# Optimization experiments

Hardware: AMD Instinct MI355X
Metric: run time of the kernel (lower is better)

The kernel has to match this reference:

```python
import jax, jax.numpy as jnp
import numpy as np

N = 20000        # nodes
E = 640000       # edges (before self-loops)
F_IN = 128
HID = 64
HEADS = 4
F_OUT = 128
G = 64           # graphs in batch
NEG_SLOPE = 0.2  # PyG GATConv leaky_relu default


def setup_inputs() -> dict:
    key = jax.random.key(0)
    ks = jax.random.split(key, 16)
    s = 0.05
    x = jax.random.normal(ks[0], (N, F_IN), jnp.float32)
    edge_index = jax.random.randint(ks[1], (2, E), 0, N, dtype=jnp.int64)
    batch = jnp.sort(jax.random.randint(ks[2], (N,), 0, G, dtype=jnp.int64))
    # layer 1: F_IN -> HID x HEADS (concat)
    W1 = jax.random.normal(ks[3], (F_IN, HEADS * HID), jnp.float32) * s
    a_src1 = jax.random.normal(ks[4], (HEADS, HID), jnp.float32) * s
    a_dst1 = jax.random.normal(ks[5], (HEADS, HID), jnp.float32) * s
    b1 = jnp.zeros((HEADS * HID,), jnp.float32)
    # layer 2: HEADS*HID -> HID x HEADS (concat)
    W2 = jax.random.normal(ks[6], (HEADS * HID, HEADS * HID), jnp.float32) * s
    a_src2 = jax.random.normal(ks[7], (HEADS, HID), jnp.float32) * s
    a_dst2 = jax.random.normal(ks[8], (HEADS, HID), jnp.float32) * s
    b2 = jnp.zeros((HEADS * HID,), jnp.float32)
    # layer 3: HEADS*HID -> F_OUT, heads=1, concat=False (mean)
    W3 = jax.random.normal(ks[9], (HEADS * HID, F_OUT), jnp.float32) * s
    a_src3 = jax.random.normal(ks[10], (1, F_OUT), jnp.float32) * s
    a_dst3 = jax.random.normal(ks[11], (1, F_OUT), jnp.float32) * s
    b3 = jnp.zeros((F_OUT,), jnp.float32)
    return dict(x=x, edge_index=edge_index, batch=batch,
                W1=W1, a_src1=a_src1, a_dst1=a_dst1, b1=b1,
                W2=W2, a_src2=a_src2, a_dst2=a_dst2, b2=b2,
                W3=W3, a_src3=a_src3, a_dst3=a_dst3, b3=b3)


def _gat_layer(x, src, dst, W, a_s, a_d, b, heads, concat):
    n = x.shape[0]
    h = (x @ W).reshape(n, heads, -1)                # [N,H,C]
    alpha_s = (h * a_s[None]).sum(-1)                # [N,H]
    alpha_d = (h * a_d[None]).sum(-1)                # [N,H]
    e = jax.nn.leaky_relu(alpha_s[src] + alpha_d[dst], NEG_SLOPE)  # [E,H]
    # segment softmax over incoming edges of each dst node
    m = jax.ops.segment_max(e, dst, num_segments=n)
    ex = jnp.exp(e - m[dst])
    denom = jax.ops.segment_sum(ex, dst, num_segments=n)
    alpha = ex / (denom[dst] + 1e-16)                # [E,H]
    out = jax.ops.segment_sum(alpha[:, :, None] * h[src], dst, num_segments=n)  # [N,H,C]
    out = out.reshape(n, -1) if concat else out.mean(axis=1)
    return out + b


def reference(x, edge_index, batch, W1, a_src1, a_dst1, b1,
              W2, a_src2, a_dst2, b2, W3, a_src3, a_dst3, b3):
    n = x.shape[0]
    # add self loops (PyG GATConv default add_self_loops=True)
    loop = jnp.arange(n, dtype=edge_index.dtype)
    src = jnp.concatenate([edge_index[0], loop])
    dst = jnp.concatenate([edge_index[1], loop])

    h = _gat_layer(x, src, dst, W1, a_src1, a_dst1, b1, HEADS, True)
    h = jax.nn.elu(h)
    h = _gat_layer(h, src, dst, W2, a_src2, a_dst2, b2, HEADS, True)
    h = jax.nn.elu(h)
    h = _gat_layer(h, src, dst, W3, a_src3, a_dst3, b3, 1, False)

    # global mean pool over graphs
    sums = jax.ops.segment_sum(h, batch, num_segments=G)
    cnts = jax.ops.segment_sum(jnp.ones((n, 1), h.dtype), batch, num_segments=G)
    graph_embedding = sums / jnp.maximum(cnts, 1.0)
    return graph_embedding, h
```

## Files before the change

kernel.cpp:

```cpp
#include <hip/hip_runtime.h>
#include <hip/hip_bf16.h>
#include <math.h>

#define N_NODES 20000
#define N_EDGES 640000
#define ET_EDGES (N_EDGES + N_NODES)
#define G_GRAPHS 64
#define NEG_SLOPE 0.2f

typedef __attribute__((ext_vector_type(8))) short s8v;
typedef __attribute__((ext_vector_type(4))) float f4v;

__device__ __forceinline__ unsigned short bf_hi(float f) {
    union { float f; unsigned int u; } c; c.f = f;
    unsigned int r = (c.u + 0x7fffu + ((c.u >> 16) & 1u)) >> 16;
    return (unsigned short)r;
}
__device__ __forceinline__ float bf_f(unsigned short h) {
    union { unsigned int u; float f; } c; c.u = ((unsigned int)h) << 16;
    return c.f;
}


__global__ void hist_dst(const int* __restrict__ ei, int* __restrict__ cnt,
                         const int* __restrict__ batch, int* __restrict__ gstart) {
    int j = blockIdx.x * blockDim.x + threadIdx.x;
    if (blockIdx.x == 0 && threadIdx.x <= G_GRAPHS) {
        int g = threadIdx.x;
        int lo = 0, hi = N_NODES;
        while (lo < hi) {
            int mid = (lo + hi) >> 1;
            if (batch[mid] < g) lo = mid + 1; else hi = mid;
        }
        gstart[g] = lo;
    }
    if (j >= ET_EDGES) return;
    int d = (j < N_EDGES) ? ei[N_EDGES + j] : (j - N_EDGES);
    atomicAdd(&cnt[d], 1);
}

__global__ __launch_bounds__(1024) void scan_rowptr(const int* __restrict__ cnt,
                                                    int* __restrict__ row_ptr) {
    __shared__ int sums[1024];
    const int n = N_NODES;
    const int CH = (n + 1023) / 1024;
    int t = threadIdx.x;
    int base = t * CH;
    int s = 0;
    for (int i = 0; i < CH; ++i) {
        int idx = base + i;
        if (idx < n) s += cnt[idx];
    }
    sums[t] = s;
    __syncthreads();
    for (int o = 1; o < 1024; o <<= 1) {
        int v = (t >= o) ? sums[t - o] : 0;
        __syncthreads();
        sums[t] += v;
        __syncthreads();
    }
    int run = (t == 0) ? 0 : sums[t - 1];
    for (int i = 0; i < CH; ++i) {
        int idx = base + i;
        if (idx < n) { row_ptr[idx] = run; run += cnt[idx]; }
    }
    if (t == 1023) row_ptr[n] = sums[1023];
}

__global__ void fill_csr(const int* __restrict__ ei, const int* __restrict__ row_ptr,
                         int* __restrict__ cur, int* __restrict__ col) {
    int j = blockIdx.x * blockDim.x + threadIdx.x;
    if (j >= ET_EDGES) return;
    int s, d;
    if (j < N_EDGES) { s = ei[j]; d = ei[N_EDGES + j]; }
    else             { s = d = j - N_EDGES; }
    int pos = row_ptr[d] + atomicAdd(&cur[d], 1);
    col[pos] = s;
}


__global__ void split_f32(const float* __restrict__ in, unsigned short* __restrict__ hi,
                          unsigned short* __restrict__ lo, int n) {
    int i = (blockIdx.x * blockDim.x + threadIdx.x) * 4;
    if (i >= n) return;
    float4 v = *(const float4*)&in[i];
    ushort4 h, l;
    h.x = bf_hi(v.x); l.x = bf_hi(v.x - bf_f(h.x));
    h.y = bf_hi(v.y); l.y = bf_hi(v.y - bf_f(h.y));
    h.z = bf_hi(v.z); l.z = bf_hi(v.z - bf_f(h.z));
    h.w = bf_hi(v.w); l.w = bf_hi(v.w - bf_f(h.w));
    *(ushort4*)&hi[i] = h;
    *(ushort4*)&lo[i] = l;
}

__global__ void wsplit(const float* __restrict__ W, unsigned short* __restrict__ th,
                       unsigned short* __restrict__ tl, int K, int Nc) {
    int idx = blockIdx.x * blockDim.x + threadIdx.x;
    if (idx >= K * Nc) return;
    int k = idx / Nc, n = idx % Nc;
    float v = W[idx];
    unsigned short h = bf_hi(v);
    th[n * K + k] = h;
    tl[n * K + k] = bf_hi(v - bf_f(h));
}


#define LDT 40

__global__ __launch_bounds__(256) void gemm_split(
        const unsigned short* __restrict__ Ah, const unsigned short* __restrict__ Al,
        const unsigned short* __restrict__ Bh, const unsigned short* __restrict__ Bl,
        float* __restrict__ C, int M, int Nc, int K) {
    __shared__ unsigned short lAh[128 * LDT];
    __shared__ unsigned short lAl[128 * LDT];
    __shared__ unsigned short lBh[64 * LDT];
    __shared__ unsigned short lBl[64 * LDT];
    int bm = blockIdx.x * 128, bn = blockIdx.y * 64;
    int t = threadIdx.x, w = t >> 6, lane = t & 63;
    int wm = (w >> 1) * 64, wn = (w & 1) * 32;

    f4v acc[4][2] = {};

    int sr = t >> 1, sk = (t & 1) << 4;
    int br = t >> 2, bk = (t & 3) << 3;
    int ar = bm + sr; if (ar >= M) ar = M - 1;
    const unsigned short* pAh = Ah + (size_t)ar * K + sk;
    const unsigned short* pAl = Al + (size_t)ar * K + sk;
    const unsigned short* pBh = Bh + (size_t)(bn + br) * K + bk;
    const unsigned short* pBl = Bl + (size_t)(bn + br) * K + bk;

    int fr = lane & 15, fk = (lane >> 4) << 3;

    for (int k0 = 0; k0 < K; k0 += 32) {
        uint4 vh0 = *(const uint4*)(pAh + k0);
        uint4 vh1 = *(const uint4*)(pAh + k0 + 8);
        uint4 vl0 = *(const uint4*)(pAl + k0);
        uint4 vl1 = *(const uint4*)(pAl + k0 + 8);
        uint4 wh  = *(const uint4*)(pBh + k0);
        uint4 wl  = *(const uint4*)(pBl + k0);
        __syncthreads();
        *(uint4*)&lAh[sr * LDT + sk]     = vh0;
        *(uint4*)&lAh[sr * LDT + sk + 8] = vh1;
        *(uint4*)&lAl[sr * LDT + sk]     = vl0;
        *(uint4*)&lAl[sr * LDT + sk + 8] = vl1;
        *(uint4*)&lBh[br * LDT + bk] = wh;
        *(uint4*)&lBl[br * LDT + bk] = wl;
        __syncthreads();

        s8v a_h[4], a_l[4], b_h[2], b_l[2];
        #pragma unroll
        for (int mi = 0; mi < 4; ++mi) {
            a_h[mi] = *(const s8v*)&lAh[(wm + mi * 16 + fr) * LDT + fk];
            a_l[mi] = *(const s8v*)&lAl[(wm + mi * 16 + fr) * LDT + fk];
        }
        #pragma unroll
        for (int nj = 0; nj < 2; ++nj) {
            b_h[nj] = *(const s8v*)&lBh[(wn + nj * 16 + fr) * LDT + fk];
            b_l[nj] = *(const s8v*)&lBl[(wn + nj * 16 + fr) * LDT + fk];
        }
        #pragma unroll
        for (int mi = 0; mi < 4; ++mi)
            #pragma unroll
            for (int nj = 0; nj < 2; ++nj) {
                acc[mi][nj] = __builtin_amdgcn_mfma_f32_16x16x32_bf16(
                    a_h[mi], b_h[nj], acc[mi][nj], 0, 0, 0);
                acc[mi][nj] = __builtin_amdgcn_mfma_f32_16x16x32_bf16(
                    a_h[mi], b_l[nj], acc[mi][nj], 0, 0, 0);
                acc[mi][nj] = __builtin_amdgcn_mfma_f32_16x16x32_bf16(
                    a_l[mi], b_h[nj], acc[mi][nj], 0, 0, 0);
            }
    }

    #pragma unroll
    for (int mi = 0; mi < 4; ++mi)
        #pragma unroll
        for (int nj = 0; nj < 2; ++nj) {
            int row0 = bm + wm + mi * 16 + (lane >> 4) * 4;
            int colc = bn + wn + nj * 16 + (lane & 15);
            #pragma unroll
            for (int q = 0; q < 4; ++q) {
                int r = row0 + q;
                if (r < M) C[(size_t)r * Nc + colc] = acc[mi][nj][q];
            }
        }
}


template <int HEADS, int C>
__global__ __launch_bounds__(256) void node_alpha2(const float* __restrict__ h,
                                                   const float* __restrict__ a_src,
                                                   const float* __restrict__ a_dst,
                                                   float* __restrict__ asT,
                                                   float* __restrict__ adT) {
    constexpr int F = HEADS * C;
    constexpr int VEC = F / 64;
    constexpr int LPH = C / VEC;
    int wid = threadIdx.x >> 6, lane = threadIdx.x & 63;
    int v = blockIdx.x * 4 + wid;
    if (v >= N_NODES) return;
    const float* hp = h + (size_t)v * F + lane * VEC;
    float ps = 0.f, pd = 0.f;
    #pragma unroll
    for (int c = 0; c < VEC; ++c) {
        float hv = hp[c];
        ps = fmaf(hv, a_src[lane * VEC + c], ps);
        pd = fmaf(hv, a_dst[lane * VEC + c], pd);
    }
    #pragma unroll
    for (int o = LPH / 2; o; o >>= 1) {
        ps += __shfl_xor(ps, o);
        pd += __shfl_xor(pd, o);
    }
    if ((lane & (LPH - 1)) == 0) {
        int head = lane / LPH;
        asT[head * N_NODES + v] = ps;
        adT[head * N_NODES + v] = pd;
    }
}


template <int NSLICE, int SCH, int F, int HEADS, bool DO_ELU, bool SPLIT>
__global__ __launch_bounds__(256) void gat_aggregate_sliced(
        const float* __restrict__ h,
        const float* __restrict__ asT,
        const float* __restrict__ adT,
        const int* __restrict__ row_ptr,
        const int* __restrict__ col,
        const float* __restrict__ bias,
        float* __restrict__ out,
        unsigned short* __restrict__ oh,
        unsigned short* __restrict__ ol) {
    constexpr int CL = SCH / 4;
    constexpr int E  = 64 / CL;
    constexpr int CPH = F / HEADS;
    __shared__ int   s_off[4][64];
    __shared__ float s_p[4][64];
    int slice = blockIdx.x & (NSLICE - 1);
    int ng = blockIdx.x >> 2;
    int wid = threadIdx.x >> 6, lane = threadIdx.x & 63;
    int v = ng * 4 + wid;
    if (v >= N_NODES) return;
    int head = (slice * SCH) / CPH;
    int eg = lane / CL, cl = lane % CL;
    int r0 = row_ptr[v], r1 = row_ptr[v + 1];
    float ad = adT[head * N_NODES + v];
    const float* asrc = asT + head * N_NODES;
    float acc[4] = {};
    float lsum = 0.f;
    const char* hb = (const char*)(h + slice * SCH + cl * 4);

#define GATHER4(gg)                                                        \
    {                                                                      \
        int k0 = ((gg) + 0) * E + eg;                                      \
        int k1 = ((gg) + 1) * E + eg;                                      \
        int k2 = ((gg) + 2) * E + eg;                                      \
        int k3 = ((gg) + 3) * E + eg;                                      \
        float p0 = s_p[wid][k0]; int o0 = s_off[wid][k0];                  \
        float p1 = s_p[wid][k1]; int o1 = s_off[wid][k1];                  \
        float p2 = s_p[wid][k2]; int o2 = s_off[wid][k2];                  \
        float p3 = s_p[wid][k3]; int o3 = s_off[wid][k3];                  \
        float4 h0 = *(const float4*)(hb + o0);                             \
        float4 h1 = *(const float4*)(hb + o1);                             \
        float4 h2 = *(const float4*)(hb + o2);                             \
        float4 h3 = *(const float4*)(hb + o3);                             \
        acc[0] = fmaf(p0, h0.x, acc[0]);                                   \
        acc[1] = fmaf(p0, h0.y, acc[1]);                                   \
        acc[2] = fmaf(p0, h0.z, acc[2]);                                   \
        acc[3] = fmaf(p0, h0.w, acc[3]);                                   \
        acc[0] = fmaf(p1, h1.x, acc[0]);                                   \
        acc[1] = fmaf(p1, h1.y, acc[1]);                                   \
        acc[2] = fmaf(p1, h1.z, acc[2]);                                   \
        acc[3] = fmaf(p1, h1.w, acc[3]);                                   \
        acc[0] = fmaf(p2, h2.x, acc[0]);                                   \
        acc[1] = fmaf(p2, h2.y, acc[1]);                                   \
        acc[2] = fmaf(p2, h2.z, acc[2]);                                   \
        acc[3] = fmaf(p2, h2.w, acc[3]);                                   \
        acc[0] = fmaf(p3, h3.x, acc[0]);                                   \
        acc[1] = fmaf(p3, h3.y, acc[1]);                                   \
        acc[2] = fmaf(p3, h3.z, acc[2]);                                   \
        acc[3] = fmaf(p3, h3.w, acc[3]);                                   \
    }

    for (int base = r0; base < r1; base += 64) {
        int j = base + lane;
        bool valid = j < r1;
        int s = col[valid ? j : r0];
        float e = asrc[s] + ad;
        e = (e > 0.f) ? e : NEG_SLOPE * e;
        float p = valid ? __expf(e) : 0.f;
        lsum += p;
        s_p[wid][lane] = p;
        s_off[wid][lane] = s * (F * 4);

        int nk = min(64, r1 - base);
        int nkg = (nk + E - 1) / E;
        int g = 0;
        for (; g + 4 <= nkg; g += 4) GATHER4(g);
        if (g < nkg) GATHER4(g);
    }
#undef GATHER4

    #pragma unroll
    for (int o = 32; o; o >>= 1) lsum += __shfl_xor(lsum, o);
    #pragma unroll
    for (int c = 0; c < 4; ++c) {
        #pragma unroll
        for (int o = CL; o < 64; o <<= 1) acc[c] += __shfl_xor(acc[c], o);
    }
    if (eg == 0) {
        float inv = 1.f / (lsum + 1e-16f);
        int ch0 = slice * SCH + cl * 4;
        float o4[4];
        #pragma unroll
        for (int c = 0; c < 4; ++c) {
            float o = acc[c] * inv + bias[ch0 + c];
            if (DO_ELU) o = (o > 0.f) ? o : expm1f(o);
            o4[c] = o;
        }
        if (SPLIT) {
            ushort4 hv, lv;
            hv.x = bf_hi(o4[0]); lv.x = bf_hi(o4[0] - bf_f(hv.x));
            hv.y = bf_hi(o4[1]); lv.y = bf_hi(o4[1] - bf_f(hv.y));
            hv.z = bf_hi(o4[2]); lv.z = bf_hi(o4[2] - bf_f(hv.z));
            hv.w = bf_hi(o4[3]); lv.w = bf_hi(o4[3] - bf_f(hv.w));
            *(ushort4*)&oh[(size_t)v * F + ch0] = hv;
            *(ushort4*)&ol[(size_t)v * F + ch0] = lv;
        } else {
            *(float4*)&out[(size_t)v * F + ch0] =
                make_float4(o4[0], o4[1], o4[2], o4[3]);
        }
    }
}


__global__ void pool_mean4(const float* __restrict__ hout, const int* __restrict__ gstart,
                           float* __restrict__ gout) {
    int g = blockIdx.x;
    int q = blockIdx.y;
    int c = threadIdx.x;
    int off = gstart[g], end = gstart[g + 1];
    float inv = 1.f / fmaxf((float)(end - off), 1.0f);
    float s = 0.f;
    for (int i = off + q; i < end; i += 4) s += hout[(size_t)i * 128 + c];
    atomicAdd(&gout[g * 128 + c], s * inv);
}


static inline size_t align_up(size_t x, size_t a) { return (x + a - 1) & ~(a - 1); }

extern "C" void kernel_launch(void* const* d_in, const int* in_sizes, int n_in,
                              void* d_out, int out_size, void* d_ws, size_t ws_size,
                              hipStream_t stream) {
    const float* x   = (const float*)d_in[0];
    const int*   ei  = (const int*)d_in[1];
    const int*   bat = (const int*)d_in[2];
    const float* W1  = (const float*)d_in[3];
    const float* as1 = (const float*)d_in[4];
    const float* ad1 = (const float*)d_in[5];
    const float* b1  = (const float*)d_in[6];
    const float* W2  = (const float*)d_in[7];
    const float* as2 = (const float*)d_in[8];
    const float* ad2 = (const float*)d_in[9];
    const float* b2  = (const float*)d_in[10];
    const float* W3  = (const float*)d_in[11];
    const float* as3 = (const float*)d_in[12];
    const float* ad3 = (const float*)d_in[13];
    const float* b3  = (const float*)d_in[14];

    float* gout = (float*)d_out;
    float* hout = (float*)d_out + G_GRAPHS * 128;

    char* w = (char*)d_ws;
    size_t o = 0;
    float* bufA = (float*)(w + o);           o = align_up(o + (size_t)N_NODES * 256 * 4, 256);
    unsigned short* Bh = (unsigned short*)(w + o); o = align_up(o + (size_t)N_NODES * 256 * 2, 256);
    unsigned short* Bl = (unsigned short*)(w + o); o = align_up(o + (size_t)N_NODES * 256 * 2, 256);
    unsigned short* xh = (unsigned short*)(w + o); o = align_up(o + (size_t)N_NODES * 128 * 2, 256);
    unsigned short* xl = (unsigned short*)(w + o); o = align_up(o + (size_t)N_NODES * 128 * 2, 256);
    unsigned short* Wt1h = (unsigned short*)(w + o); o = align_up(o + (size_t)256 * 128 * 2, 256);
    unsigned short* Wt1l = (unsigned short*)(w + o); o = align_up(o + (size_t)256 * 128 * 2, 256);
    unsigned short* Wt2h = (unsigned short*)(w + o); o = align_up(o + (size_t)256 * 256 * 2, 256);
    unsigned short* Wt2l = (unsigned short*)(w + o); o = align_up(o + (size_t)256 * 256 * 2, 256);
    unsigned short* Wt3h = (unsigned short*)(w + o); o = align_up(o + (size_t)128 * 256 * 2, 256);
    unsigned short* Wt3l = (unsigned short*)(w + o); o = align_up(o + (size_t)128 * 256 * 2, 256);
    float* asv  = (float*)(w + o); o = align_up(o + (size_t)N_NODES * 4 * 4, 256);
    float* adv  = (float*)(w + o); o = align_up(o + (size_t)N_NODES * 4 * 4, 256);
    int* row_ptr = (int*)(w + o);  o = align_up(o + (size_t)(N_NODES + 1) * 4, 256);
    int* col     = (int*)(w + o);  o = align_up(o + (size_t)ET_EDGES * 4, 256);
    int* cnt     = (int*)(w + o);  o += (size_t)N_NODES * 4;
    int* cur     = (int*)(w + o);  o = align_up(o + (size_t)N_NODES * 4, 256);
    int* gstart  = (int*)(w + o);  o = align_up(o + (size_t)(G_GRAPHS + 1) * 4, 256);

    hipMemsetAsync(cnt, 0, (size_t)N_NODES * 8, stream);
    hipMemsetAsync(gout, 0, (size_t)G_GRAPHS * 128 * 4, stream);
    hist_dst<<<(ET_EDGES + 255) / 256, 256, 0, stream>>>(ei, cnt, bat, gstart);
    scan_rowptr<<<1, 1024, 0, stream>>>(cnt, row_ptr);
    fill_csr<<<(ET_EDGES + 255) / 256, 256, 0, stream>>>(ei, row_ptr, cur, col);
    split_f32<<<(N_NODES * 128 / 4 + 255) / 256, 256, 0, stream>>>(x, xh, xl, N_NODES * 128);
    wsplit<<<(128 * 256 + 255) / 256, 256, 0, stream>>>(W1, Wt1h, Wt1l, 128, 256);
    wsplit<<<(256 * 256 + 255) / 256, 256, 0, stream>>>(W2, Wt2h, Wt2l, 256, 256);
    wsplit<<<(256 * 128 + 255) / 256, 256, 0, stream>>>(W3, Wt3h, Wt3l, 256, 128);

    int gm = (N_NODES + 127) / 128;
    int nb = (N_NODES + 3) / 4;
    int nbs = nb * 4;

    gemm_split<<<dim3(gm, 4), 256, 0, stream>>>(xh, xl, Wt1h, Wt1l, bufA, N_NODES, 256, 128);
    node_alpha2<4, 64><<<nb, 256, 0, stream>>>(bufA, as1, ad1, asv, adv);
    gat_aggregate_sliced<4, 64, 256, 4, true, true><<<nbs, 256, 0, stream>>>(
        bufA, asv, adv, row_ptr, col, b1, nullptr, Bh, Bl);

    gemm_split<<<dim3(gm, 4), 256, 0, stream>>>(Bh, Bl, Wt2h, Wt2l, bufA, N_NODES, 256, 256);
    node_alpha2<4, 64><<<nb, 256, 0, stream>>>(bufA, as2, ad2, asv, adv);
    gat_aggregate_sliced<4, 64, 256, 4, true, true><<<nbs, 256, 0, stream>>>(
        bufA, asv, adv, row_ptr, col, b2, nullptr, Bh, Bl);

    gemm_split<<<dim3(gm, 2), 256, 0, stream>>>(Bh, Bl, Wt3h, Wt3l, bufA, N_NODES, 128, 256);
    node_alpha2<1, 128><<<nb, 256, 0, stream>>>(bufA, as3, ad3, asv, adv);
    gat_aggregate_sliced<4, 32, 128, 1, false, false><<<nbs, 256, 0, stream>>>(
        bufA, asv, adv, row_ptr, col, b3, hout, nullptr, nullptr);

    pool_mean4<<<dim3(G_GRAPHS, 4), 128, 0, stream>>>(hout, gstart, gout);
}
```

Before: 433.2 us.

## Split GAT aggregation into 8 channel slices with a fully unrolled 64-edge gather

The aggregation kernels now use 8 channel slices instead of 4, so each block handles half as many channels and twice as many blocks are launched. The per-chunk gather loop is fully unrolled over all 64 shared-memory slots, always issuing CL loads, instead of looping only over the valid edges. Edge probability and offset are packed into one int2 in shared memory. The column reads and the bf16 split-output stores become nontemporal. The aim is more memory-level parallelism and fewer loop-control branches. In exchange, each node's column indices, attention logits and exponentials are recomputed in twice as many blocks, and padded slots issue redundant gathers of the first source row.

```diff
diff --git a/kernel.cpp b/kernel.cpp
--- a/kernel.cpp
+++ b/kernel.cpp
@@ -233,10 +233,9 @@
     constexpr int CL = SCH / 4;
     constexpr int E  = 64 / CL;
     constexpr int CPH = F / HEADS;
-    __shared__ int   s_off[4][64];
-    __shared__ float s_p[4][64];
+    __shared__ int2 s_po[4][64];
     int slice = blockIdx.x & (NSLICE - 1);
-    int ng = blockIdx.x >> 2;
+    int ng = blockIdx.x / NSLICE;
     int wid = threadIdx.x >> 6, lane = threadIdx.x & 63;
     int v = ng * 4 + wid;
     if (v >= N_NODES) return;
@@ -249,56 +248,31 @@
     float lsum = 0.f;
     const char* hb = (const char*)(h + slice * SCH + cl * 4);
 
-#define GATHER4(gg)                                                        \
-    {                                                                      \
-        int k0 = ((gg) + 0) * E + eg;                                      \
-        int k1 = ((gg) + 1) * E + eg;                                      \
-        int k2 = ((gg) + 2) * E + eg;                                      \
-        int k3 = ((gg) + 3) * E + eg;                                      \
-        float p0 = s_p[wid][k0]; int o0 = s_off[wid][k0];                  \
-        float p1 = s_p[wid][k1]; int o1 = s_off[wid][k1];                  \
-        float p2 = s_p[wid][k2]; int o2 = s_off[wid][k2];                  \
-        float p3 = s_p[wid][k3]; int o3 = s_off[wid][k3];                  \
-        float4 h0 = *(const float4*)(hb + o0);                             \
-        float4 h1 = *(const float4*)(hb + o1);                             \
-        float4 h2 = *(const float4*)(hb + o2);                             \
-        float4 h3 = *(const float4*)(hb + o3);                             \
-        acc[0] = fmaf(p0, h0.x, acc[0]);                                   \
-        acc[1] = fmaf(p0, h0.y, acc[1]);                                   \
-        acc[2] = fmaf(p0, h0.z, acc[2]);                                   \
-        acc[3] = fmaf(p0, h0.w, acc[3]);                                   \
-        acc[0] = fmaf(p1, h1.x, acc[0]);                                   \
-        acc[1] = fmaf(p1, h1.y, acc[1]);                                   \
-        acc[2] = fmaf(p1, h1.z, acc[2]);                                   \
-        acc[3] = fmaf(p1, h1.w, acc[3]);                                   \
-        acc[0] = fmaf(p2, h2.x, acc[0]);                                   \
-        acc[1] = fmaf(p2, h2.y, acc[1]);                                   \
-        acc[2] = fmaf(p2, h2.z, acc[2]);                                   \
-        acc[3] = fmaf(p2, h2.w, acc[3]);                                   \
-        acc[0] = fmaf(p3, h3.x, acc[0]);                                   \
-        acc[1] = fmaf(p3, h3.y, acc[1]);                                   \
-        acc[2] = fmaf(p3, h3.z, acc[2]);                                   \
-        acc[3] = fmaf(p3, h3.w, acc[3]);                                   \
-    }
-
     for (int base = r0; base < r1; base += 64) {
         int j = base + lane;
         bool valid = j < r1;
-        int s = col[valid ? j : r0];
+        int s = __builtin_nontemporal_load(&col[valid ? j : r0]);
         float e = asrc[s] + ad;
         e = (e > 0.f) ? e : NEG_SLOPE * e;
         float p = valid ? __expf(e) : 0.f;
         lsum += p;
-        s_p[wid][lane] = p;
-        s_off[wid][lane] = s * (F * 4);
-
-        int nk = min(64, r1 - base);
-        int nkg = (nk + E - 1) / E;
-        int g = 0;
-        for (; g + 4 <= nkg; g += 4) GATHER4(g);
-        if (g < nkg) GATHER4(g);
-    }
-#undef GATHER4
+        s_po[wid][lane] = make_int2(s * (F * 4), __float_as_int(p));
+
+        int2 po[CL];
+        #pragma unroll
+        for (int g = 0; g < CL; ++g) po[g] = s_po[wid][g * E + eg];
+        float4 hv[CL];
+        #pragma unroll
+        for (int g = 0; g < CL; ++g) hv[g] = *(const float4*)(hb + po[g].x);
+        #pragma unroll
+        for (int g = 0; g < CL; ++g) {
+            float pk = __int_as_float(po[g].y);
+            acc[0] = fmaf(pk, hv[g].x, acc[0]);
+            acc[1] = fmaf(pk, hv[g].y, acc[1]);
+            acc[2] = fmaf(pk, hv[g].z, acc[2]);
+            acc[3] = fmaf(pk, hv[g].w, acc[3]);
+        }
+    }
 
     #pragma unroll
     for (int o = 32; o; o >>= 1) lsum += __shfl_xor(lsum, o);
@@ -318,13 +292,16 @@
             o4[c] = o;
         }
         if (SPLIT) {
-            ushort4 hv, lv;
-            hv.x = bf_hi(o4[0]); lv.x = bf_hi(o4[0] - bf_f(hv.x));
-            hv.y = bf_hi(o4[1]); lv.y = bf_hi(o4[1] - bf_f(hv.y));
-            hv.z = bf_hi(o4[2]); lv.z = bf_hi(o4[2] - bf_f(hv.z));
-            hv.w = bf_hi(o4[3]); lv.w = bf_hi(o4[3] - bf_f(hv.w));
-            *(ushort4*)&oh[(size_t)v * F + ch0] = hv;
-            *(ushort4*)&ol[(size_t)v * F + ch0] = lv;
+            ushort4 hv4, lv4;
+            hv4.x = bf_hi(o4[0]); lv4.x = bf_hi(o4[0] - bf_f(hv4.x));
+            hv4.y = bf_hi(o4[1]); lv4.y = bf_hi(o4[1] - bf_f(hv4.y));
+            hv4.z = bf_hi(o4[2]); lv4.z = bf_hi(o4[2] - bf_f(hv4.z));
+            hv4.w = bf_hi(o4[3]); lv4.w = bf_hi(o4[3] - bf_f(hv4.w));
+            unsigned long long hvu, lvu;
+            __builtin_memcpy(&hvu, &hv4, 8);
+            __builtin_memcpy(&lvu, &lv4, 8);
+            __builtin_nontemporal_store(hvu, (unsigned long long*)&oh[(size_t)v * F + ch0]);
+            __builtin_nontemporal_store(lvu, (unsigned long long*)&ol[(size_t)v * F + ch0]);
         } else {
             *(float4*)&out[(size_t)v * F + ch0] =
                 make_float4(o4[0], o4[1], o4[2], o4[3]);
@@ -403,21 +380,21 @@
 
     int gm = (N_NODES + 127) / 128;
     int nb = (N_NODES + 3) / 4;
-    int nbs = nb * 4;
+    int nbs = nb * 8;
 
     gemm_split<<<dim3(gm, 4), 256, 0, stream>>>(xh, xl, Wt1h, Wt1l, bufA, N_NODES, 256, 128);
     node_alpha2<4, 64><<<nb, 256, 0, stream>>>(bufA, as1, ad1, asv, adv);
-    gat_aggregate_sliced<4, 64, 256, 4, true, true><<<nbs, 256, 0, stream>>>(
+    gat_aggregate_sliced<8, 32, 256, 4, true, true><<<nbs, 256, 0, stream>>>(
         bufA, asv, adv, row_ptr, col, b1, nullptr, Bh, Bl);
 
     gemm_split<<<dim3(gm, 4), 256, 0, stream>>>(Bh, Bl, Wt2h, Wt2l, bufA, N_NODES, 256, 256);
     node_alpha2<4, 64><<<nb, 256, 0, stream>>>(bufA, as2, ad2, asv, adv);
-    gat_aggregate_sliced<4, 64, 256, 4, true, true><<<nbs, 256, 0, stream>>>(
+    gat_aggregate_sliced<8, 32, 256, 4, true, true><<<nbs, 256, 0, stream>>>(
         bufA, asv, adv, row_ptr, col, b2, nullptr, Bh, Bl);
 
     gemm_split<<<dim3(gm, 2), 256, 0, stream>>>(Bh, Bl, Wt3h, Wt3l, bufA, N_NODES, 128, 256);
     node_alpha2<1, 128><<<nb, 256, 0, stream>>>(bufA, as3, ad3, asv, adv);
-    gat_aggregate_sliced<4, 32, 128, 1, false, false><<<nbs, 256, 0, stream>>>(
+    gat_aggregate_sliced<8, 16, 128, 1, false, false><<<nbs, 256, 0, stream>>>(
         bufA, asv, adv, row_ptr, col, b3, hout, nullptr, nullptr);
 
     pool_mean4<<<dim3(G_GRAPHS, 4), 128, 0, stream>>>(hout, gstart, gout);
```

Measured after the change: 568.9 us. +31.3%, slower.

## Precompute edge softmax weights in separate pass, fuse prep kernels, unroll gather by 8

Applied to the files above, without the earlier changes.

Folds the x/W bf16 splitting and the memsets into one prep kernel, which cuts launch count. Adds a per-layer edge_alpha pass that computes the exp attention weights and per-node denominators once per edge and stores them in a [head, E] buffer. Before this, each of the 4 channel slices recomputed them. The aggregate kernel now reads those precomputed weights and uses an 8-wide gather unroll. The cost is an extra kernel per layer and extra global traffic for the pex buffer (about 10 MB written and read back per layer).

```diff
diff --git a/kernel.cpp b/kernel.cpp
--- a/kernel.cpp
+++ b/kernel.cpp
@@ -79,29 +79,63 @@
 }
 
 
-__global__ void split_f32(const float* __restrict__ in, unsigned short* __restrict__ hi,
-                          unsigned short* __restrict__ lo, int n) {
-    int i = (blockIdx.x * blockDim.x + threadIdx.x) * 4;
-    if (i >= n) return;
-    float4 v = *(const float4*)&in[i];
-    ushort4 h, l;
-    h.x = bf_hi(v.x); l.x = bf_hi(v.x - bf_f(h.x));
-    h.y = bf_hi(v.y); l.y = bf_hi(v.y - bf_f(h.y));
-    h.z = bf_hi(v.z); l.z = bf_hi(v.z - bf_f(h.z));
-    h.w = bf_hi(v.w); l.w = bf_hi(v.w - bf_f(h.w));
-    *(ushort4*)&hi[i] = h;
-    *(ushort4*)&lo[i] = l;
-}
-
-__global__ void wsplit(const float* __restrict__ W, unsigned short* __restrict__ th,
-                       unsigned short* __restrict__ tl, int K, int Nc) {
+__global__ void prep_split(const float* __restrict__ x,
+                           const float* __restrict__ W1, const float* __restrict__ W2,
+                           const float* __restrict__ W3,
+                           unsigned short* __restrict__ xh, unsigned short* __restrict__ xl,
+                           unsigned short* __restrict__ w1h, unsigned short* __restrict__ w1l,
+                           unsigned short* __restrict__ w2h, unsigned short* __restrict__ w2l,
+                           unsigned short* __restrict__ w3h, unsigned short* __restrict__ w3l,
+                           int* __restrict__ cntcur, float* __restrict__ gout) {
     int idx = blockIdx.x * blockDim.x + threadIdx.x;
-    if (idx >= K * Nc) return;
-    int k = idx / Nc, n = idx % Nc;
-    float v = W[idx];
-    unsigned short h = bf_hi(v);
-    th[n * K + k] = h;
-    tl[n * K + k] = bf_hi(v - bf_f(h));
+    if (idx < 640000) {
+        int i = idx * 4;
+        float4 v = *(const float4*)&x[i];
+        ushort4 h, l;
+        h.x = bf_hi(v.x); l.x = bf_hi(v.x - bf_f(h.x));
+        h.y = bf_hi(v.y); l.y = bf_hi(v.y - bf_f(h.y));
+        h.z = bf_hi(v.z); l.z = bf_hi(v.z - bf_f(h.z));
+        h.w = bf_hi(v.w); l.w = bf_hi(v.w - bf_f(h.w));
+        *(ushort4*)&xh[i] = h;
+        *(ushort4*)&xl[i] = l;
+        return;
+    }
+    idx -= 640000;
+    if (idx < 32768) {
+        int k = idx / 256, n = idx % 256;
+        float v = W1[idx];
+        unsigned short h = bf_hi(v);
+        w1h[n * 128 + k] = h;
+        w1l[n * 128 + k] = bf_hi(v - bf_f(h));
+        return;
+    }
+    idx -= 32768;
+    if (idx < 65536) {
+        int k = idx / 256, n = idx % 256;
+        float v = W2[idx];
+        unsigned short h = bf_hi(v);
+        w2h[n * 256 + k] = h;
+        w2l[n * 256 + k] = bf_hi(v - bf_f(h));
+        return;
+    }
+    idx -= 65536;
+    if (idx < 32768) {
+        int k = idx / 128, n = idx % 128;
+        float v = W3[idx];
+        unsigned short h = bf_hi(v);
+        w3h[n * 256 + k] = h;
+        w3l[n * 256 + k] = bf_hi(v - bf_f(h));
+        return;
+    }
+    idx -= 32768;
+    if (idx < 10000) {
+        *(int4*)&cntcur[idx * 4] = make_int4(0, 0, 0, 0);
+        return;
+    }
+    idx -= 10000;
+    if (idx < 2048) {
+        *(float4*)&gout[idx * 4] = make_float4(0.f, 0.f, 0.f, 0.f);
+    }
 }
 
 
@@ -187,11 +221,11 @@
 
 
 template <int HEADS, int C>
-__global__ __launch_bounds__(256) void node_alpha2(const float* __restrict__ h,
+__global__ __launch_bounds__(256) void node_alpha3(const float* __restrict__ h,
                                                    const float* __restrict__ a_src,
                                                    const float* __restrict__ a_dst,
-                                                   float* __restrict__ asT,
-                                                   float* __restrict__ adT) {
+                                                   float* __restrict__ asi,
+                                                   float* __restrict__ adi) {
     constexpr int F = HEADS * C;
     constexpr int VEC = F / 64;
     constexpr int LPH = C / VEC;
@@ -213,17 +247,67 @@
     }
     if ((lane & (LPH - 1)) == 0) {
         int head = lane / LPH;
-        asT[head * N_NODES + v] = ps;
-        adT[head * N_NODES + v] = pd;
-    }
-}
-
-
-template <int NSLICE, int SCH, int F, int HEADS, bool DO_ELU, bool SPLIT>
-__global__ __launch_bounds__(256) void gat_aggregate_sliced(
+        asi[v * HEADS + head] = ps;
+        adi[v * HEADS + head] = pd;
+    }
+}
+
+
+template <int H>
+__global__ __launch_bounds__(256) void edge_alpha2(
+        const float* __restrict__ asi,
+        const float* __restrict__ adi,
+        const int* __restrict__ row_ptr,
+        const int* __restrict__ col,
+        float* __restrict__ pex,
+        float* __restrict__ dn) {
+    int wid = threadIdx.x >> 6, lane = threadIdx.x & 63;
+    int v = blockIdx.x * 4 + wid;
+    if (v >= N_NODES) return;
+    int r0 = row_ptr[v], r1 = row_ptr[v + 1];
+    float adh[H];
+    #pragma unroll
+    for (int t = 0; t < H; ++t) adh[t] = adi[v * H + t];
+    float ls[H] = {};
+    for (int base = r0; base < r1; base += 64) {
+        int j = base + lane;
+        bool valid = j < r1;
+        int s = col[valid ? j : r0];
+        if (H == 4) {
+            float4 a4 = *(const float4*)&asi[(size_t)s * 4];
+            float as_[4] = { a4.x, a4.y, a4.z, a4.w };
+            #pragma unroll
+            for (int t = 0; t < 4; ++t) {
+                float e = as_[t] + adh[t];
+                e = (e > 0.f) ? e : NEG_SLOPE * e;
+                float p = valid ? __expf(e) : 0.f;
+                ls[t] += p;
+                if (valid) pex[(size_t)t * ET_EDGES + j] = p;
+            }
+        } else {
+            float e = asi[s] + adh[0];
+            e = (e > 0.f) ? e : NEG_SLOPE * e;
+            float p = valid ? __expf(e) : 0.f;
+            ls[0] += p;
+            if (valid) pex[j] = p;
+        }
+    }
+    #pragma unroll
+    for (int t = 0; t < H; ++t)
+        #pragma unroll
+        for (int o = 32; o; o >>= 1) ls[t] += __shfl_xor(ls[t], o);
+    if (lane == 0) {
+        #pragma unroll
+        for (int t = 0; t < H; ++t) dn[v * H + t] = ls[t];
+    }
+}
+
+
+template <int SCH, int F, int H, bool DO_ELU, bool SPLIT>
+__global__ __launch_bounds__(256) void gat_aggregate4(
         const float* __restrict__ h,
-        const float* __restrict__ asT,
-        const float* __restrict__ adT,
+        const float* __restrict__ pex,
+        const float* __restrict__ dn,
         const int* __restrict__ row_ptr,
         const int* __restrict__ col,
         const float* __restrict__ bias,
@@ -232,10 +316,10 @@
         unsigned short* __restrict__ ol) {
     constexpr int CL = SCH / 4;
     constexpr int E  = 64 / CL;
-    constexpr int CPH = F / HEADS;
+    constexpr int CPH = F / H;
     __shared__ int   s_off[4][64];
     __shared__ float s_p[4][64];
-    int slice = blockIdx.x & (NSLICE - 1);
+    int slice = blockIdx.x & 3;
     int ng = blockIdx.x >> 2;
     int wid = threadIdx.x >> 6, lane = threadIdx.x & 63;
     int v = ng * 4 + wid;
@@ -243,10 +327,8 @@
     int head = (slice * SCH) / CPH;
     int eg = lane / CL, cl = lane % CL;
     int r0 = row_ptr[v], r1 = row_ptr[v + 1];
-    float ad = adT[head * N_NODES + v];
-    const float* asrc = asT + head * N_NODES;
+    const float* pp = pex + (size_t)head * ET_EDGES;
     float acc[4] = {};
-    float lsum = 0.f;
     const char* hb = (const char*)(h + slice * SCH + cl * 4);
 
 #define GATHER4(gg)                                                        \
@@ -281,34 +363,53 @@
         acc[3] = fmaf(p3, h3.w, acc[3]);                                   \
     }
 
+#define GATHER8(gg)                                                        \
+    {                                                                      \
+        int kk[8]; float pw[8]; int ow[8];                                 \
+        _Pragma("unroll")                                                  \
+        for (int u = 0; u < 8; ++u) kk[u] = ((gg) + u) * E + eg;           \
+        _Pragma("unroll")                                                  \
+        for (int u = 0; u < 8; ++u) { pw[u] = s_p[wid][kk[u]];             \
+                                      ow[u] = s_off[wid][kk[u]]; }         \
+        float4 hw[8];                                                      \
+        _Pragma("unroll")                                                  \
+        for (int u = 0; u < 8; ++u) hw[u] = *(const float4*)(hb + ow[u]);  \
+        _Pragma("unroll")                                                  \
+        for (int u = 0; u < 8; ++u) {                                      \
+            acc[0] = fmaf(pw[u], hw[u].x, acc[0]);                         \
+            acc[1] = fmaf(pw[u], hw[u].y, acc[1]);                         \
+            acc[2] = fmaf(pw[u], hw[u].z, acc[2]);                         \
+            acc[3] = fmaf(pw[u], hw[u].w, acc[3]);                         \
+        }                                                                  \
+    }
+
     for (int base = r0; base < r1; base += 64) {
         int j = base + lane;
         bool valid = j < r1;
         int s = col[valid ? j : r0];
-        float e = asrc[s] + ad;
-        e = (e > 0.f) ? e : NEG_SLOPE * e;
-        float p = valid ? __expf(e) : 0.f;
-        lsum += p;
+        float p = valid ? pp[j] : 0.f;
         s_p[wid][lane] = p;
         s_off[wid][lane] = s * (F * 4);
 
         int nk = min(64, r1 - base);
         int nkg = (nk + E - 1) / E;
         int g = 0;
-        for (; g + 4 <= nkg; g += 4) GATHER4(g);
-        if (g < nkg) GATHER4(g);
+        for (; g + 8 <= nkg; g += 8) GATHER8(g);
+        if (g < nkg) {
+            GATHER4(g);
+            if (g + 4 < nkg) GATHER4(g + 4);
+        }
     }
 #undef GATHER4
-
-    #pragma unroll
-    for (int o = 32; o; o >>= 1) lsum += __shfl_xor(lsum, o);
+#undef GATHER8
+
     #pragma unroll
     for (int c = 0; c < 4; ++c) {
         #pragma unroll
         for (int o = CL; o < 64; o <<= 1) acc[c] += __shfl_xor(acc[c], o);
     }
     if (eg == 0) {
-        float inv = 1.f / (lsum + 1e-16f);
+        float inv = 1.f / (dn[v * H + head] + 1e-16f);
         int ch0 = slice * SCH + cl * 4;
         float o4[4];
         #pragma unroll
@@ -317,14 +418,14 @@
             if (DO_ELU) o = (o > 0.f) ? o : expm1f(o);
             o4[c] = o;
         }
-        if (SPLIT) {
-            ushort4 hv, lv;
-            hv.x = bf_hi(o4[0]); lv.x = bf_hi(o4[0] - bf_f(hv.x));
-            hv.y = bf_hi(o4[1]); lv.y = bf_hi(o4[1] - bf_f(hv.y));
-            hv.z = bf_hi(o4[2]); lv.z = bf_hi(o4[2] - bf_f(hv.z));
-            hv.w = bf_hi(o4[3]); lv.w = bf_hi(o4[3] - bf_f(hv.w));
-            *(ushort4*)&oh[(size_t)v * F + ch0] = hv;
-            *(ushort4*)&ol[(size_t)v * F + ch0] = lv;
+        if constexpr (SPLIT) {
+            ushort4 hv4, lv4;
+            hv4.x = bf_hi(o4[0]); lv4.x = bf_hi(o4[0] - bf_f(hv4.x));
+            hv4.y = bf_hi(o4[1]); lv4.y = bf_hi(o4[1] - bf_f(hv4.y));
+            hv4.z = bf_hi(o4[2]); lv4.z = bf_hi(o4[2] - bf_f(hv4.z));
+            hv4.w = bf_hi(o4[3]); lv4.w = bf_hi(o4[3] - bf_f(hv4.w));
+            *(ushort4*)&oh[(size_t)v * F + ch0] = hv4;
+            *(ushort4*)&ol[(size_t)v * F + ch0] = lv4;
         } else {
             *(float4*)&out[(size_t)v * F + ch0] =
                 make_float4(o4[0], o4[1], o4[2], o4[3]);
@@ -385,40 +486,44 @@
     unsigned short* Wt3l = (unsigned short*)(w + o); o = align_up(o + (size_t)128 * 256 * 2, 256);
     float* asv  = (float*)(w + o); o = align_up(o + (size_t)N_NODES * 4 * 4, 256);
     float* adv  = (float*)(w + o); o = align_up(o + (size_t)N_NODES * 4 * 4, 256);
+    float* pex  = (float*)(w + o); o = align_up(o + (size_t)ET_EDGES * 4 * 4, 256);
+    float* dnv  = (float*)(w + o); o = align_up(o + (size_t)N_NODES * 4 * 4, 256);
     int* row_ptr = (int*)(w + o);  o = align_up(o + (size_t)(N_NODES + 1) * 4, 256);
     int* col     = (int*)(w + o);  o = align_up(o + (size_t)ET_EDGES * 4, 256);
     int* cnt     = (int*)(w + o);  o += (size_t)N_NODES * 4;
     int* cur     = (int*)(w + o);  o = align_up(o + (size_t)N_NODES * 4, 256);
     int* gstart  = (int*)(w + o);  o = align_up(o + (size_t)(G_GRAPHS + 1) * 4, 256);
 
-    hipMemsetAsync(cnt, 0, (size_t)N_NODES * 8, stream);
-    hipMemsetAsync(gout, 0, (size_t)G_GRAPHS * 128 * 4, stream);
+    {
+        int total = 640000 + 32768 + 65536 + 32768 + 10000 + 2048;
+        prep_split<<<(total + 255) / 256, 256, 0, stream>>>(
+            x, W1, W2, W3, xh, xl, Wt1h, Wt1l, Wt2h, Wt2l, Wt3h, Wt3l, cnt, gout);
+    }
     hist_dst<<<(ET_EDGES + 255) / 256, 256, 0, stream>>>(ei, cnt, bat, gstart);
     scan_rowptr<<<1, 1024, 0, stream>>>(cnt, row_ptr);
     fill_csr<<<(ET_EDGES + 255) / 256, 256, 0, stream>>>(ei, row_ptr, cur, col);
-    split_f32<<<(N_NODES * 128 / 4 + 255) / 256, 256, 0, stream>>>(x, xh, xl, N_NODES * 128);
-    wsplit<<<(128 * 256 + 255) / 256, 256, 0, stream>>>(W1, Wt1h, Wt1l, 128, 256);
-    wsplit<<<(256 * 256 + 255) / 256, 256, 0, stream>>>(W2, Wt2h, Wt2l, 256, 256);
-    wsplit<<<(256 * 128 + 255) / 256, 256, 0, stream>>>(W3, Wt3h, Wt3l, 256, 128);
 
     int gm = (N_NODES + 127) / 128;
     int nb = (N_NODES + 3) / 4;
     int nbs = nb * 4;
 
     gemm_split<<<dim3(gm, 4), 256, 0, stream>>>(xh, xl, Wt1h, Wt1l, bufA, N_NODES, 256, 128);
-    node_alpha2<4, 64><<<nb, 256, 0, stream>>>(bufA, as1, ad1, asv, adv);
-    gat_aggregate_sliced<4, 64, 256, 4, true, true><<<nbs, 256, 0, stream>>>(
-        bufA, asv, adv, row_ptr, col, b1, nullptr, Bh, Bl);
+    node_alpha3<4, 64><<<nb, 256, 0, stream>>>(bufA, as1, ad1, asv, adv);
+    edge_alpha2<4><<<nb, 256, 0, stream>>>(asv, adv, row_ptr, col, pex, dnv);
+    gat_aggregate4<64, 256, 4, true, true><<<nbs, 256, 0, stream>>>(
+        bufA, pex, dnv, row_ptr, col, b1, nullptr, Bh, Bl);
 
     gemm_split<<<dim3(gm, 4), 256, 0, stream>>>(Bh, Bl, Wt2h, Wt2l, bufA, N_NODES, 256, 256);
-    node_alpha2<4, 64><<<nb, 256, 0, stream>>>(bufA, as2, ad2, asv, adv);
-    gat_aggregate_sliced<4, 64, 256, 4, true, true><<<nbs, 256, 0, stream>>>(
-        bufA, asv, adv, row_ptr, col, b2, nullptr, Bh, Bl);
+    node_alpha3<4, 64><<<nb, 256, 0, stream>>>(bufA, as2, ad2, asv, adv);
+    edge_alpha2<4><<<nb, 256, 0, stream>>>(asv, adv, row_ptr, col, pex, dnv);
+    gat_aggregate4<64, 256, 4, true, true><<<nbs, 256, 0, stream>>>(
+        bufA, pex, dnv, row_ptr, col, b2, nullptr, Bh, Bl);
 
     gemm_split<<<dim3(gm, 2), 256, 0, stream>>>(Bh, Bl, Wt3h, Wt3l, bufA, N_NODES, 128, 256);
-    node_alpha2<1, 128><<<nb, 256, 0, stream>>>(bufA, as3, ad3, asv, adv);
-    gat_aggregate_sliced<4, 32, 128, 1, false, false><<<nbs, 256, 0, stream>>>(
-        bufA, asv, adv, row_ptr, col, b3, hout, nullptr, nullptr);
+    node_alpha3<1, 128><<<nb, 256, 0, stream>>>(bufA, as3, ad3, asv, adv);
+    edge_alpha2<1><<<nb, 256, 0, stream>>>(asv, adv, row_ptr, col, pex, dnv);
+    gat_aggregate4<32, 128, 1, false, false><<<nbs, 256, 0, stream>>>(
+        bufA, pex, dnv, row_ptr, col, b3, hout, nullptr, nullptr);
 
     pool_mean4<<<dim3(G_GRAPHS, 4), 128, 0, stream>>>(hout, gstart, gout);
 }
```

After: 447.5 us. +3.3%, slower.
